# Performance work log

Measured on AMD Instinct MI355X. Metric: run time of the kernel, lower is better.

Reference implementation:

```python
import jax, jax.numpy as jnp
import numpy as np

SCALE = 8.0  # sqrt(head_dim=64)
B, H, S, D = 2, 16, 2048, 64


def setup_inputs() -> dict:
    key = jax.random.key(0)
    kq, kk, kv = jax.random.split(key, 3)
    query = jax.random.normal(kq, (B, H, S, D), dtype=jnp.float32)
    key_t = jax.random.normal(kk, (B, H, S, D), dtype=jnp.float32)
    value = jax.random.normal(kv, (B, H, S, D), dtype=jnp.float32)
    # causal target mask (B, 1, S, S); 0 = masked
    mask = jnp.broadcast_to(jnp.tril(jnp.ones((S, S), dtype=jnp.int32)), (B, 1, S, S))
    return {"query": query, "key": key_t, "value": value, "mask": mask}


def reference(query, key, value, mask):
    # scores: (B, H, S, S)
    scores = jnp.einsum("bhqd,bhkd->bhqk", query, key) / SCALE
    scores = jnp.where(mask == 0, -jnp.inf, scores)
    attn = jax.nn.softmax(scores, axis=-1)  # dropout_rate=0.0 -> identity
    return jnp.einsum("bhqk,bhkd->bhqd", attn, value)
```

## Files before the change

### kernel.cpp

```cpp
#include <hip/hip_runtime.h>
#include <hip/hip_bf16.h>


#define S_ 2048
#define D_ 64
#define NBH 32

typedef __bf16 bf16x8 __attribute__((ext_vector_type(8)));
typedef float f32x4 __attribute__((ext_vector_type(4)));
typedef unsigned short u16x4 __attribute__((ext_vector_type(4)));
typedef unsigned short u16x8 __attribute__((ext_vector_type(8)));

static __device__ __forceinline__ unsigned short f2bf(float f) {
    union { float f; unsigned u; } v; v.f = f;
    unsigned r = v.u + 0x7FFFu + ((v.u >> 16) & 1u);
    return (unsigned short)(r >> 16);
}

__global__ __launch_bounds__(256)
void prep_k(const float* __restrict__ K, unsigned short* __restrict__ Kbf) {
    #pragma unroll
    for (int i = 0; i < 2; ++i) {
        const int p = blockIdx.x * 512 + i * 256 + threadIdx.x;
        float4 x = reinterpret_cast<const float4*>(K)[p];
        u16x4 o = { f2bf(x.x), f2bf(x.y), f2bf(x.z), f2bf(x.w) };
        reinterpret_cast<u16x4*>(Kbf)[p] = o;
    }
}

__global__ __launch_bounds__(256)
void prep_v(const float* __restrict__ V, unsigned short* __restrict__ Vt) {
    __shared__ float Vl[64][65];
    const int bh = blockIdx.x >> 5;
    const int kvbase = (blockIdx.x & 31) << 6;
    const float* Vb = V + (size_t)bh * S_ * D_ + (size_t)kvbase * D_;
    #pragma unroll
    for (int i = 0; i < 4; ++i) {
        const int flat = i * 1024 + threadIdx.x * 4;
        const int kv = flat >> 6, d = flat & 63;
        float4 x = *reinterpret_cast<const float4*>(Vb + kv * D_ + d);
        Vl[kv][d] = x.x; Vl[kv][d + 1] = x.y; Vl[kv][d + 2] = x.z; Vl[kv][d + 3] = x.w;
    }
    __syncthreads();
    unsigned short* Vo = Vt + (size_t)bh * D_ * S_;
    #pragma unroll
    for (int i = 0; i < 2; ++i) {
        const int p = i * 256 + threadIdx.x;
        const int d = p >> 3, c = p & 7;
        u16x8 o;
        #pragma unroll
        for (int j = 0; j < 8; ++j) o[j] = f2bf(Vl[c * 8 + j][d]);
        *reinterpret_cast<u16x8*>(Vo + d * S_ + kvbase + c * 8) = o;
    }
}

__global__ __launch_bounds__(256)
void attn_fwd2(const float* __restrict__ Q, const unsigned short* __restrict__ Kbf,
               const unsigned short* __restrict__ Vtbf, float* __restrict__ O) {
    const int tid  = threadIdx.x;
    const int wave = tid >> 6;
    const int lane = tid & 63;
    const int lg   = lane >> 4;
    const int lr   = lane & 15;

    const int wg   = blockIdx.x;
    const int bh   = wg & 31;
    const int qblk = 31 - (wg >> 5);
    const int q0   = qblk << 6;

    const float*          Qb = Q    + (size_t)bh * S_ * D_;
    const unsigned short* Kg = Kbf  + (size_t)bh * S_ * D_;
    const unsigned short* Vg = Vtbf + (size_t)bh * D_ * S_;
    float*                Ob = O    + (size_t)bh * S_ * D_;

    __shared__ __align__(16) unsigned short Kl[2][4096];
    __shared__ __align__(16) unsigned short Vl[2][4096];
    __shared__ unsigned short Pl[4][16][72];

    const float qscale = 0.18033688011112042f;
    bf16x8 qa[2];
    {
        const int qrow = q0 + wave * 16 + lr;
        #pragma unroll
        for (int kt = 0; kt < 2; ++kt) {
            const float* src = Qb + qrow * D_ + kt * 32 + lg * 8;
            float4 x = *reinterpret_cast<const float4*>(src);
            float4 y = *reinterpret_cast<const float4*>(src + 4);
            union { unsigned short u[8]; bf16x8 v; } pk;
            pk.u[0] = f2bf(x.x * qscale); pk.u[1] = f2bf(x.y * qscale);
            pk.u[2] = f2bf(x.z * qscale); pk.u[3] = f2bf(x.w * qscale);
            pk.u[4] = f2bf(y.x * qscale); pk.u[5] = f2bf(y.y * qscale);
            pk.u[6] = f2bf(y.z * qscale); pk.u[7] = f2bf(y.w * qscale);
            qa[kt] = pk.v;
        }
    }

    f32x4 oacc[4];
    #pragma unroll
    for (int i = 0; i < 4; ++i) oacc[i] = {0.f, 0.f, 0.f, 0.f};
    float m_[4], l_[4];
    #pragma unroll
    for (int r = 0; r < 4; ++r) { m_[r] = -__builtin_inff(); l_[r] = 0.f; }

    const int nkv = (q0 >> 6) + 1;

    auto stage = [&](int buf, int t) {
        #pragma unroll
        for (int i = 0; i < 2; ++i) {
            const int p   = wave * 128 + i * 64 + lane;
            const int row = p >> 3, c = p & 7;
            const int sc  = c ^ (row & 7);
            const unsigned short* gk = Kg + (size_t)(t * 64 + row) * 64 + sc * 8;
            __builtin_amdgcn_global_load_lds(
                (const __attribute__((address_space(1))) void*)gk,
                (__attribute__((address_space(3))) void*)&Kl[buf][(wave * 128 + i * 64) * 8],
                16, 0, 0);
            const unsigned short* gv = Vg + (size_t)row * S_ + t * 64 + sc * 8;
            __builtin_amdgcn_global_load_lds(
                (const __attribute__((address_space(1))) void*)gv,
                (__attribute__((address_space(3))) void*)&Vl[buf][(wave * 128 + i * 64) * 8],
                16, 0, 0);
        }
    };

    stage(0, 0);
    __syncthreads();

    for (int t = 0; t < nkv; ++t) {
        if (t + 1 < nkv) stage((t + 1) & 1, t + 1);
        const unsigned short* Kb_ = Kl[t & 1];
        const unsigned short* Vb_ = Vl[t & 1];
        const int kvbase = t << 6;

        f32x4 sacc[4];
        #pragma unroll
        for (int kvt = 0; kvt < 4; ++kvt) {
            sacc[kvt] = {0.f, 0.f, 0.f, 0.f};
            #pragma unroll
            for (int kt = 0; kt < 2; ++kt) {
                bf16x8 kb = *reinterpret_cast<const bf16x8*>(
                    &Kb_[((kvt * 16 + lr) * 8 + ((kt * 4 + lg) ^ (lr & 7))) * 8]);
                sacc[kvt] = __builtin_amdgcn_mfma_f32_16x16x32_bf16(qa[kt], kb, sacc[kvt], 0, 0, 0);
            }
        }

        if (t == nkv - 1) {
            #pragma unroll
            for (int kvt = 0; kvt < 4; ++kvt) {
                const int kvg = kvbase + kvt * 16 + lr;
                #pragma unroll
                for (int r = 0; r < 4; ++r) {
                    const int qg = q0 + wave * 16 + lg * 4 + r;
                    if (kvg > qg) sacc[kvt][r] = -__builtin_inff();
                }
            }
        }

        float al[4];
        #pragma unroll
        for (int r = 0; r < 4; ++r) {
            float v = fmaxf(fmaxf(sacc[0][r], sacc[1][r]), fmaxf(sacc[2][r], sacc[3][r]));
            #pragma unroll
            for (int off = 1; off < 16; off <<= 1)
                v = fmaxf(v, __shfl_xor(v, off, 16));
            const float mn = fmaxf(m_[r], v);
            al[r] = __builtin_amdgcn_exp2f(m_[r] - mn);
            m_[r] = mn;
        }
        #pragma unroll
        for (int kvt = 0; kvt < 4; ++kvt)
            #pragma unroll
            for (int r = 0; r < 4; ++r)
                sacc[kvt][r] = __builtin_amdgcn_exp2f(sacc[kvt][r] - m_[r]);
        #pragma unroll
        for (int r = 0; r < 4; ++r) {
            float s = (sacc[0][r] + sacc[1][r]) + (sacc[2][r] + sacc[3][r]);
            #pragma unroll
            for (int off = 1; off < 16; off <<= 1)
                s += __shfl_xor(s, off, 16);
            l_[r] = l_[r] * al[r] + s;
            #pragma unroll
            for (int dt = 0; dt < 4; ++dt) oacc[dt][r] *= al[r];
        }

        #pragma unroll
        for (int kvt = 0; kvt < 4; ++kvt)
            #pragma unroll
            for (int r = 0; r < 4; ++r)
                Pl[wave][lg * 4 + r][kvt * 16 + lr] = f2bf(sacc[kvt][r]);

        bf16x8 pa0 = *reinterpret_cast<const bf16x8*>(&Pl[wave][lr][lg * 8]);
        bf16x8 pa1 = *reinterpret_cast<const bf16x8*>(&Pl[wave][lr][32 + lg * 8]);

        #pragma unroll
        for (int dt = 0; dt < 4; ++dt) {
            bf16x8 vb0 = *reinterpret_cast<const bf16x8*>(
                &Vb_[((dt * 16 + lr) * 8 + ((0 * 4 + lg) ^ (lr & 7))) * 8]);
            oacc[dt] = __builtin_amdgcn_mfma_f32_16x16x32_bf16(pa0, vb0, oacc[dt], 0, 0, 0);
            bf16x8 vb1 = *reinterpret_cast<const bf16x8*>(
                &Vb_[((dt * 16 + lr) * 8 + ((1 * 4 + lg) ^ (lr & 7))) * 8]);
            oacc[dt] = __builtin_amdgcn_mfma_f32_16x16x32_bf16(pa1, vb1, oacc[dt], 0, 0, 0);
        }

        __syncthreads();
    }

    #pragma unroll
    for (int r = 0; r < 4; ++r) {
        const int qrow = q0 + wave * 16 + lg * 4 + r;
        const float inv = 1.0f / l_[r];
        #pragma unroll
        for (int dt = 0; dt < 4; ++dt)
            Ob[(size_t)qrow * D_ + dt * 16 + lr] = oacc[dt][r] * inv;
    }
}

extern "C" void kernel_launch(void* const* d_in, const int* in_sizes, int n_in,
                              void* d_out, int out_size, void* d_ws, size_t ws_size,
                              hipStream_t stream) {
    const float* Q = (const float*)d_in[0];
    const float* K = (const float*)d_in[1];
    const float* V = (const float*)d_in[2];
    float* O = (float*)d_out;

    unsigned short* Kbf = (unsigned short*)d_ws;
    unsigned short* Vt  = Kbf + (size_t)NBH * S_ * D_;

    hipLaunchKernelGGL(prep_k,    dim3(2048), dim3(256), 0, stream, K, Kbf);
    hipLaunchKernelGGL(prep_v,    dim3(1024), dim3(256), 0, stream, V, Vt);
    hipLaunchKernelGGL(attn_fwd2, dim3(1024), dim3(256), 0, stream, Q, Kbf, Vt, O);
}
```

Before: 164.9 us.

## Pair causal query blocks per workgroup, fuse K/V prep, lazy rescale, MFMA row sums

Merges the K and V bf16 conversion kernels into one launch and uses native bf16 conversion. The attention kernel now handles two query blocks per workgroup (a long one and its complementary short one), halving the grid to balance causal work across workgroups. It also skips online-softmax rescaling unless the row max grows by more than a threshold, computes row sums with an MFMA against a ones vector, and raises wave priority around MFMA sections. The lazy rescale relies on the exp2 range staying bounded, and the grid of 512 may underfill the GPU's compute units.

After: 159.2 us. 3.5% less time.

```diff
diff --git a/kernel.cpp b/kernel.cpp
--- a/kernel.cpp
+++ b/kernel.cpp
@@ -11,28 +11,27 @@
 typedef unsigned short u16x4 __attribute__((ext_vector_type(4)));
 typedef unsigned short u16x8 __attribute__((ext_vector_type(8)));
 
-static __device__ __forceinline__ unsigned short f2bf(float f) {
-    union { float f; unsigned u; } v; v.f = f;
-    unsigned r = v.u + 0x7FFFu + ((v.u >> 16) & 1u);
-    return (unsigned short)(r >> 16);
+static __device__ __forceinline__ unsigned short bfb(float f) {
+    return __builtin_bit_cast(unsigned short, (__bf16)f);
 }
 
 __global__ __launch_bounds__(256)
-void prep_k(const float* __restrict__ K, unsigned short* __restrict__ Kbf) {
-    #pragma unroll
-    for (int i = 0; i < 2; ++i) {
-        const int p = blockIdx.x * 512 + i * 256 + threadIdx.x;
-        float4 x = reinterpret_cast<const float4*>(K)[p];
-        u16x4 o = { f2bf(x.x), f2bf(x.y), f2bf(x.z), f2bf(x.w) };
-        reinterpret_cast<u16x4*>(Kbf)[p] = o;
-    }
-}
-
-__global__ __launch_bounds__(256)
-void prep_v(const float* __restrict__ V, unsigned short* __restrict__ Vt) {
-    __shared__ float Vl[64][65];
+void prep_kv(const float* __restrict__ K, const float* __restrict__ V,
+             unsigned short* __restrict__ Kbf, unsigned short* __restrict__ Vt) {
     const int bh = blockIdx.x >> 5;
     const int kvbase = (blockIdx.x & 31) << 6;
+
+    const float* Ks = K + (size_t)bh * S_ * D_ + (size_t)kvbase * D_;
+    unsigned short* Kd = Kbf + (size_t)bh * S_ * D_ + (size_t)kvbase * D_;
+    #pragma unroll
+    for (int i = 0; i < 4; ++i) {
+        const int p = i * 256 + threadIdx.x;
+        float4 x = reinterpret_cast<const float4*>(Ks)[p];
+        u16x4 o = { bfb(x.x), bfb(x.y), bfb(x.z), bfb(x.w) };
+        reinterpret_cast<u16x4*>(Kd)[p] = o;
+    }
+
+    __shared__ float Vl[64][65];
     const float* Vb = V + (size_t)bh * S_ * D_ + (size_t)kvbase * D_;
     #pragma unroll
     for (int i = 0; i < 4; ++i) {
@@ -49,13 +48,13 @@
         const int d = p >> 3, c = p & 7;
         u16x8 o;
         #pragma unroll
-        for (int j = 0; j < 8; ++j) o[j] = f2bf(Vl[c * 8 + j][d]);
+        for (int j = 0; j < 8; ++j) o[j] = bfb(Vl[c * 8 + j][d]);
         *reinterpret_cast<u16x8*>(Vo + d * S_ + kvbase + c * 8) = o;
     }
 }
 
 __global__ __launch_bounds__(256)
-void attn_fwd2(const float* __restrict__ Q, const unsigned short* __restrict__ Kbf,
+void attn_fwd3(const float* __restrict__ Q, const unsigned short* __restrict__ Kbf,
                const unsigned short* __restrict__ Vtbf, float* __restrict__ O) {
     const int tid  = threadIdx.x;
     const int wave = tid >> 6;
@@ -63,10 +62,9 @@
     const int lg   = lane >> 4;
     const int lr   = lane & 15;
 
-    const int wg   = blockIdx.x;
-    const int bh   = wg & 31;
-    const int qblk = 31 - (wg >> 5);
-    const int q0   = qblk << 6;
+    const int wg = blockIdx.x;
+    const int bh = wg & 31;
+    const int pr = wg >> 5;
 
     const float*          Qb = Q    + (size_t)bh * S_ * D_;
     const unsigned short* Kg = Kbf  + (size_t)bh * S_ * D_;
@@ -77,32 +75,9 @@
     __shared__ __align__(16) unsigned short Vl[2][4096];
     __shared__ unsigned short Pl[4][16][72];
 
-    const float qscale = 0.18033688011112042f;
-    bf16x8 qa[2];
-    {
-        const int qrow = q0 + wave * 16 + lr;
-        #pragma unroll
-        for (int kt = 0; kt < 2; ++kt) {
-            const float* src = Qb + qrow * D_ + kt * 32 + lg * 8;
-            float4 x = *reinterpret_cast<const float4*>(src);
-            float4 y = *reinterpret_cast<const float4*>(src + 4);
-            union { unsigned short u[8]; bf16x8 v; } pk;
-            pk.u[0] = f2bf(x.x * qscale); pk.u[1] = f2bf(x.y * qscale);
-            pk.u[2] = f2bf(x.z * qscale); pk.u[3] = f2bf(x.w * qscale);
-            pk.u[4] = f2bf(y.x * qscale); pk.u[5] = f2bf(y.y * qscale);
-            pk.u[6] = f2bf(y.z * qscale); pk.u[7] = f2bf(y.w * qscale);
-            qa[kt] = pk.v;
-        }
-    }
-
-    f32x4 oacc[4];
-    #pragma unroll
-    for (int i = 0; i < 4; ++i) oacc[i] = {0.f, 0.f, 0.f, 0.f};
-    float m_[4], l_[4];
-    #pragma unroll
-    for (int r = 0; r < 4; ++r) { m_[r] = -__builtin_inff(); l_[r] = 0.f; }
-
-    const int nkv = (q0 >> 6) + 1;
+    bf16x8 ones;
+    #pragma unroll
+    for (int i = 0; i < 8; ++i) ones[i] = (__bf16)1.0f;
 
     auto stage = [&](int buf, int t) {
         #pragma unroll
@@ -113,106 +88,148 @@
             const unsigned short* gk = Kg + (size_t)(t * 64 + row) * 64 + sc * 8;
             __builtin_amdgcn_global_load_lds(
                 (const __attribute__((address_space(1))) void*)gk,
-                (__attribute__((address_space(3))) void*)&Kl[buf][(wave * 128 + i * 64) * 8],
-                16, 0, 0);
+                (__attribute__((address_space(3))) void*)&Kl[buf][p * 8], 16, 0, 0);
             const unsigned short* gv = Vg + (size_t)row * S_ + t * 64 + sc * 8;
             __builtin_amdgcn_global_load_lds(
                 (const __attribute__((address_space(1))) void*)gv,
-                (__attribute__((address_space(3))) void*)&Vl[buf][(wave * 128 + i * 64) * 8],
-                16, 0, 0);
+                (__attribute__((address_space(3))) void*)&Vl[buf][p * 8], 16, 0, 0);
         }
     };
 
-    stage(0, 0);
+    const float qscale = 0.18033688011112042f;
+
+    auto run_pass = [&](int q0) {
+        bf16x8 qa[2];
+        {
+            const int qrow = q0 + wave * 16 + lr;
+            #pragma unroll
+            for (int kt = 0; kt < 2; ++kt) {
+                const float* src = Qb + qrow * D_ + kt * 32 + lg * 8;
+                float4 x = *reinterpret_cast<const float4*>(src);
+                float4 y = *reinterpret_cast<const float4*>(src + 4);
+                union { unsigned short u[8]; bf16x8 v; } pk;
+                pk.u[0] = bfb(x.x * qscale); pk.u[1] = bfb(x.y * qscale);
+                pk.u[2] = bfb(x.z * qscale); pk.u[3] = bfb(x.w * qscale);
+                pk.u[4] = bfb(y.x * qscale); pk.u[5] = bfb(y.y * qscale);
+                pk.u[6] = bfb(y.z * qscale); pk.u[7] = bfb(y.w * qscale);
+                qa[kt] = pk.v;
+            }
+        }
+
+        f32x4 oacc[4];
+        #pragma unroll
+        for (int i = 0; i < 4; ++i) oacc[i] = {0.f, 0.f, 0.f, 0.f};
+        float m_[4], l_[4];
+        #pragma unroll
+        for (int r = 0; r < 4; ++r) { m_[r] = -__builtin_inff(); l_[r] = 0.f; }
+
+        const int nkv = (q0 >> 6) + 1;
+        stage(0, 0);
+        __syncthreads();
+
+        for (int t = 0; t < nkv; ++t) {
+            if (t + 1 < nkv) stage((t + 1) & 1, t + 1);
+            const unsigned short* Kb_ = Kl[t & 1];
+            const unsigned short* Vb_ = Vl[t & 1];
+            const int kvbase = t << 6;
+
+            f32x4 sacc[4];
+            __builtin_amdgcn_s_setprio(1);
+            #pragma unroll
+            for (int kvt = 0; kvt < 4; ++kvt) {
+                sacc[kvt] = {0.f, 0.f, 0.f, 0.f};
+                #pragma unroll
+                for (int kt = 0; kt < 2; ++kt) {
+                    bf16x8 kb = *reinterpret_cast<const bf16x8*>(
+                        &Kb_[((kvt * 16 + lr) * 8 + ((kt * 4 + lg) ^ (lr & 7))) * 8]);
+                    sacc[kvt] = __builtin_amdgcn_mfma_f32_16x16x32_bf16(qa[kt], kb, sacc[kvt], 0, 0, 0);
+                }
+            }
+            __builtin_amdgcn_s_setprio(0);
+
+            if (t == nkv - 1) {
+                #pragma unroll
+                for (int kvt = 0; kvt < 4; ++kvt) {
+                    const int kvg = kvbase + kvt * 16 + lr;
+                    #pragma unroll
+                    for (int r = 0; r < 4; ++r) {
+                        const int qg = q0 + wave * 16 + lg * 4 + r;
+                        if (kvg > qg) sacc[kvt][r] = -__builtin_inff();
+                    }
+                }
+            }
+
+            float pm[4];
+            bool resc = false;
+            #pragma unroll
+            for (int r = 0; r < 4; ++r) {
+                float v = fmaxf(fmaxf(sacc[0][r], sacc[1][r]), fmaxf(sacc[2][r], sacc[3][r]));
+                #pragma unroll
+                for (int off = 1; off < 16; off <<= 1)
+                    v = fmaxf(v, __shfl_xor(v, off, 16));
+                pm[r] = v;
+                resc = resc || (v > m_[r] + 8.0f);
+            }
+            if (__any((int)resc)) {
+                #pragma unroll
+                for (int r = 0; r < 4; ++r) {
+                    const float mn = fmaxf(m_[r], pm[r]);
+                    const float al = __builtin_amdgcn_exp2f(m_[r] - mn);
+                    m_[r] = mn;
+                    l_[r] *= al;
+                    #pragma unroll
+                    for (int dt = 0; dt < 4; ++dt) oacc[dt][r] *= al;
+                }
+            }
+            #pragma unroll
+            for (int kvt = 0; kvt < 4; ++kvt)
+                #pragma unroll
+                for (int r = 0; r < 4; ++r)
+                    sacc[kvt][r] = __builtin_amdgcn_exp2f(sacc[kvt][r] - m_[r]);
+
+            #pragma unroll
+            for (int kvt = 0; kvt < 4; ++kvt)
+                #pragma unroll
+                for (int r = 0; r < 4; ++r)
+                    Pl[wave][lg * 4 + r][kvt * 16 + lr] = bfb(sacc[kvt][r]);
+
+            bf16x8 pa0 = *reinterpret_cast<const bf16x8*>(&Pl[wave][lr][lg * 8]);
+            bf16x8 pa1 = *reinterpret_cast<const bf16x8*>(&Pl[wave][lr][32 + lg * 8]);
+
+            f32x4 ssum = {0.f, 0.f, 0.f, 0.f};
+            __builtin_amdgcn_s_setprio(1);
+            #pragma unroll
+            for (int dt = 0; dt < 4; ++dt) {
+                bf16x8 vb0 = *reinterpret_cast<const bf16x8*>(
+                    &Vb_[((dt * 16 + lr) * 8 + ((0 * 4 + lg) ^ (lr & 7))) * 8]);
+                oacc[dt] = __builtin_amdgcn_mfma_f32_16x16x32_bf16(pa0, vb0, oacc[dt], 0, 0, 0);
+                bf16x8 vb1 = *reinterpret_cast<const bf16x8*>(
+                    &Vb_[((dt * 16 + lr) * 8 + ((1 * 4 + lg) ^ (lr & 7))) * 8]);
+                oacc[dt] = __builtin_amdgcn_mfma_f32_16x16x32_bf16(pa1, vb1, oacc[dt], 0, 0, 0);
+            }
+            ssum = __builtin_amdgcn_mfma_f32_16x16x32_bf16(pa0, ones, ssum, 0, 0, 0);
+            ssum = __builtin_amdgcn_mfma_f32_16x16x32_bf16(pa1, ones, ssum, 0, 0, 0);
+            __builtin_amdgcn_s_setprio(0);
+
+            #pragma unroll
+            for (int r = 0; r < 4; ++r) l_[r] += ssum[r];
+
+            __syncthreads();
+        }
+
+        #pragma unroll
+        for (int r = 0; r < 4; ++r) {
+            const int qrow = q0 + wave * 16 + lg * 4 + r;
+            const float inv = 1.0f / l_[r];
+            #pragma unroll
+            for (int dt = 0; dt < 4; ++dt)
+                Ob[(size_t)qrow * D_ + dt * 16 + lr] = oacc[dt][r] * inv;
+        }
+    };
+
+    run_pass((31 - pr) << 6);
     __syncthreads();
-
-    for (int t = 0; t < nkv; ++t) {
-        if (t + 1 < nkv) stage((t + 1) & 1, t + 1);
-        const unsigned short* Kb_ = Kl[t & 1];
-        const unsigned short* Vb_ = Vl[t & 1];
-        const int kvbase = t << 6;
-
-        f32x4 sacc[4];
-        #pragma unroll
-        for (int kvt = 0; kvt < 4; ++kvt) {
-            sacc[kvt] = {0.f, 0.f, 0.f, 0.f};
-            #pragma unroll
-            for (int kt = 0; kt < 2; ++kt) {
-                bf16x8 kb = *reinterpret_cast<const bf16x8*>(
-                    &Kb_[((kvt * 16 + lr) * 8 + ((kt * 4 + lg) ^ (lr & 7))) * 8]);
-                sacc[kvt] = __builtin_amdgcn_mfma_f32_16x16x32_bf16(qa[kt], kb, sacc[kvt], 0, 0, 0);
-            }
-        }
-
-        if (t == nkv - 1) {
-            #pragma unroll
-            for (int kvt = 0; kvt < 4; ++kvt) {
-                const int kvg = kvbase + kvt * 16 + lr;
-                #pragma unroll
-                for (int r = 0; r < 4; ++r) {
-                    const int qg = q0 + wave * 16 + lg * 4 + r;
-                    if (kvg > qg) sacc[kvt][r] = -__builtin_inff();
-                }
-            }
-        }
-
-        float al[4];
-        #pragma unroll
-        for (int r = 0; r < 4; ++r) {
-            float v = fmaxf(fmaxf(sacc[0][r], sacc[1][r]), fmaxf(sacc[2][r], sacc[3][r]));
-            #pragma unroll
-            for (int off = 1; off < 16; off <<= 1)
-                v = fmaxf(v, __shfl_xor(v, off, 16));
-            const float mn = fmaxf(m_[r], v);
-            al[r] = __builtin_amdgcn_exp2f(m_[r] - mn);
-            m_[r] = mn;
-        }
-        #pragma unroll
-        for (int kvt = 0; kvt < 4; ++kvt)
-            #pragma unroll
-            for (int r = 0; r < 4; ++r)
-                sacc[kvt][r] = __builtin_amdgcn_exp2f(sacc[kvt][r] - m_[r]);
-        #pragma unroll
-        for (int r = 0; r < 4; ++r) {
-            float s = (sacc[0][r] + sacc[1][r]) + (sacc[2][r] + sacc[3][r]);
-            #pragma unroll
-            for (int off = 1; off < 16; off <<= 1)
-                s += __shfl_xor(s, off, 16);
-            l_[r] = l_[r] * al[r] + s;
-            #pragma unroll
-            for (int dt = 0; dt < 4; ++dt) oacc[dt][r] *= al[r];
-        }
-
-        #pragma unroll
-        for (int kvt = 0; kvt < 4; ++kvt)
-            #pragma unroll
-            for (int r = 0; r < 4; ++r)
-                Pl[wave][lg * 4 + r][kvt * 16 + lr] = f2bf(sacc[kvt][r]);
-
-        bf16x8 pa0 = *reinterpret_cast<const bf16x8*>(&Pl[wave][lr][lg * 8]);
-        bf16x8 pa1 = *reinterpret_cast<const bf16x8*>(&Pl[wave][lr][32 + lg * 8]);
-
-        #pragma unroll
-        for (int dt = 0; dt < 4; ++dt) {
-            bf16x8 vb0 = *reinterpret_cast<const bf16x8*>(
-                &Vb_[((dt * 16 + lr) * 8 + ((0 * 4 + lg) ^ (lr & 7))) * 8]);
-            oacc[dt] = __builtin_amdgcn_mfma_f32_16x16x32_bf16(pa0, vb0, oacc[dt], 0, 0, 0);
-            bf16x8 vb1 = *reinterpret_cast<const bf16x8*>(
-                &Vb_[((dt * 16 + lr) * 8 + ((1 * 4 + lg) ^ (lr & 7))) * 8]);
-            oacc[dt] = __builtin_amdgcn_mfma_f32_16x16x32_bf16(pa1, vb1, oacc[dt], 0, 0, 0);
-        }
-
-        __syncthreads();
-    }
-
-    #pragma unroll
-    for (int r = 0; r < 4; ++r) {
-        const int qrow = q0 + wave * 16 + lg * 4 + r;
-        const float inv = 1.0f / l_[r];
-        #pragma unroll
-        for (int dt = 0; dt < 4; ++dt)
-            Ob[(size_t)qrow * D_ + dt * 16 + lr] = oacc[dt][r] * inv;
-    }
+    run_pass(pr << 6);
 }
 
 extern "C" void kernel_launch(void* const* d_in, const int* in_sizes, int n_in,
@@ -226,7 +243,6 @@
     unsigned short* Kbf = (unsigned short*)d_ws;
     unsigned short* Vt  = Kbf + (size_t)NBH * S_ * D_;
 
-    hipLaunchKernelGGL(prep_k,    dim3(2048), dim3(256), 0, stream, K, Kbf);
-    hipLaunchKernelGGL(prep_v,    dim3(1024), dim3(256), 0, stream, V, Vt);
-    hipLaunchKernelGGL(attn_fwd2, dim3(1024), dim3(256), 0, stream, Q, Kbf, Vt, O);
-}
+    hipLaunchKernelGGL(prep_kv,   dim3(1024), dim3(256), 0, stream, K, V, Kbf, Vt);
+    hipLaunchKernelGGL(attn_fwd3, dim3(512),  dim3(256), 0, stream, Q, Kbf, Vt, O);
+}
```
